# Kernel tuning notes

Measured on AMD Instinct MI355X. Metric: run time of the kernel, lower is better.

Reference implementation:

```python
import jax, jax.numpy as jnp
import numpy as np

N = 5000      # nodes per event (hardcoded in PFNet7.forward)
BIN = 100     # LSH bin_size
K = 16        # kNN per node within bin
SLOPE = 0.01  # LeakyReLU default negative slope


def _mlp(x, W1, b1, W2, b2, W3, b3):
    h = jax.nn.leaky_relu(x @ W1 + b1, SLOPE)
    h = jax.nn.leaky_relu(h @ W2 + b2, SLOPE)
    return h @ W3 + b3


def _build_graph_lsh(x, codebook):
    # x: [N, F]. Faithful vectorized version of GraphBuildingLSH (batch=1).
    n_bins = N // BIN                                   # 50
    mul = x @ codebook[:, : n_bins // 2]                # [N, 25]
    cmul = jnp.concatenate([mul, -mul], axis=-1)        # [N, 50]
    bin_idx = jnp.argmax(cmul, axis=-1)                 # [N]
    bins_split = jnp.argsort(bin_idx).reshape(n_bins, BIN)  # [nb, BIN]
    pts = x[bins_split]                                 # [nb, BIN, F]
    dm = jax.nn.sigmoid(jnp.einsum('pif,pjf->pij', pts, pts))  # [nb, BIN, BIN]
    vals, inds = jax.lax.top_k(dm, K)                   # [nb, BIN, K]
    src = jnp.broadcast_to(bins_split[:, :, None], inds.shape).reshape(-1)
    dst = jnp.take_along_axis(bins_split, inds.reshape(n_bins, -1), axis=1).reshape(-1)
    val = vals.reshape(-1)                              # [nb*BIN*K] = 80000 edges
    return src, dst, val


def _gcn_conv(x, W, b, src, dst, ew):
    # PyG GCNConv: add self-loops (weight 1), symmetric normalization, aggregate at col.
    n = x.shape[0]
    loop = jnp.arange(n)
    row = jnp.concatenate([src, loop])
    col = jnp.concatenate([dst, loop])
    w = jnp.concatenate([ew, jnp.ones((n,), x.dtype)])
    deg = jax.ops.segment_sum(w, col, num_segments=n)
    dis = jnp.where(deg > 0, deg ** -0.5, 0.0)
    norm = dis[row] * w * dis[col]
    h = x @ W
    out = jax.ops.segment_sum(norm[:, None] * h[row], col, num_segments=n)
    return out + b


def _graph_conv(x, Wrel, brel, Wroot, src, dst, ew):
    # PyG GraphConv(aggr='add'): lin_rel(sum_j w_ij x_j) + lin_root(x)
    agg = jax.ops.segment_sum(ew[:, None] * x[src], dst, num_segments=x.shape[0])
    return agg @ Wrel + brel + x @ Wroot


def setup_inputs() -> dict:
    key = jax.random.key(0)
    ks = jax.random.split(key, 24)
    f32 = jnp.float32
    d = {
        'x': jax.random.normal(ks[0], (N, 12), f32),
        'ygen_id': jax.random.normal(ks[1], (N, 6), f32),
        'ygen': jax.random.normal(ks[2], (N, 6), f32),
        'codebook': jax.random.normal(ks[3], (12, 100), f32),
        # nn1: 12 -> 125 -> 125 -> 12
        'nn1_W1': jax.random.normal(ks[4], (12, 125), f32) * 0.1,
        'nn1_b1': jnp.zeros((125,), f32),
        'nn1_W2': jax.random.normal(ks[5], (125, 125), f32) * 0.1,
        'nn1_b2': jnp.zeros((125,), f32),
        'nn1_W3': jax.random.normal(ks[6], (125, 12), f32) * 0.1,
        'nn1_b3': jnp.zeros((12,), f32),
        # GCNConv: 12 -> 32
        'gcn_W': jax.random.normal(ks[7], (12, 32), f32) * 0.1,
        'gcn_b': jnp.zeros((32,), f32),
        # GraphConv: 32 -> 32
        'gc_Wrel': jax.random.normal(ks[8], (32, 32), f32) * 0.1,
        'gc_brel': jnp.zeros((32,), f32),
        'gc_Wroot': jax.random.normal(ks[9], (32, 32), f32) * 0.1,
        # nn2: 32 -> 125 -> 125 -> 6
        'nn2_W1': jax.random.normal(ks[10], (32, 125), f32) * 0.1,
        'nn2_b1': jnp.zeros((125,), f32),
        'nn2_W2': jax.random.normal(ks[11], (125, 125), f32) * 0.1,
        'nn2_b2': jnp.zeros((125,), f32),
        'nn2_W3': jax.random.normal(ks[12], (125, 6), f32) * 0.1,
        'nn2_b3': jnp.zeros((6,), f32),
        # nn3: 38 -> 125 -> 125 -> 6
        'nn3_W1': jax.random.normal(ks[13], (38, 125), f32) * 0.1,
        'nn3_b1': jnp.zeros((125,), f32),
        'nn3_W2': jax.random.normal(ks[14], (125, 125), f32) * 0.1,
        'nn3_b2': jnp.zeros((125,), f32),
        'nn3_W3': jax.random.normal(ks[15], (125, 6), f32) * 0.1,
        'nn3_b3': jnp.zeros((6,), f32),
    }
    return d


def reference(x, ygen_id, ygen, codebook,
              nn1_W1, nn1_b1, nn1_W2, nn1_b2, nn1_W3, nn1_b3,
              gcn_W, gcn_b, gc_Wrel, gc_brel, gc_Wroot,
              nn2_W1, nn2_b1, nn2_W2, nn2_b2, nn2_W3, nn2_b3,
              nn3_W1, nn3_b1, nn3_W2, nn3_b2, nn3_W3, nn3_b3):
    h = _mlp(x, nn1_W1, nn1_b1, nn1_W2, nn1_b2, nn1_W3, nn1_b3)   # [N, 12]
    src, dst, ew = _build_graph_lsh(h, codebook)
    h = jax.nn.leaky_relu(h, SLOPE)
    h = _gcn_conv(h, gcn_W, gcn_b, src, dst, ew)                   # [N, 32]
    h = _graph_conv(h, gc_Wrel, gc_brel, gc_Wroot, src, dst, ew)
    h = jax.nn.leaky_relu(h, SLOPE)
    cand_ids = _mlp(h, nn2_W1, nn2_b1, nn2_W2, nn2_b2, nn2_W3, nn2_b3)
    cand_p4 = _mlp(jnp.concatenate([h, cand_ids], axis=-1),
                   nn3_W1, nn3_b1, nn3_W2, nn3_b2, nn3_W3, nn3_b3)
    return (cand_ids, cand_p4, ygen_id, ygen)
```

## Files before the change

kernel.cpp:

```cpp
#include <hip/hip_runtime.h>
#include <math.h>

#define NN 5000
#define NBINS 50
#define BINSZ 100
#define KNN 16
#define BPAD 104
#define MROWS 112
#define NB 20

typedef _Float16 half8 __attribute__((ext_vector_type(8)));

__device__ __forceinline__ float lrelu(float x){ return x >= 0.f ? x : 0.01f*x; }

__global__ __launch_bounds__(640) void nn1_kernel(
    const float* __restrict__ x,
    const float* __restrict__ W1, const float* __restrict__ b1,
    const float* __restrict__ W2, const float* __restrict__ b2,
    const float* __restrict__ W3, const float* __restrict__ b3,
    const float* __restrict__ cb,
    const float4* __restrict__ ygen_id4, const float4* __restrict__ ygen4,
    float4* __restrict__ out4,
    float* __restrict__ h_out, int* __restrict__ bin_idx)
{
    __shared__ __align__(16) float sW[18628];
    __shared__ __align__(16) float bufX[240];
    __shared__ __align__(16) float bufA[2500];
    __shared__ __align__(16) float bufB[2500];
    __shared__ __align__(16) float sCB[300];
    int tid = threadIdx.x;
    int n0 = blockIdx.x * NB;
    int g = tid >> 7, j = tid & 127;
    float acc[4];

    if (tid >= 576 && tid < 636) {
        int gI = blockIdx.x * 60 + (tid - 576);
        out4[15000 + gI] = (gI < 7500) ? ygen_id4[gI] : ygen4[gI - 7500];
    }
    if (tid < 60) {
        float4 v = ((const float4*)(x + n0 * 12))[tid];
        int e = tid * 4;
        bufX[(e % 12) * NB + (e / 12)] = v.x;
        bufX[((e + 1) % 12) * NB + ((e + 1) / 12)] = v.y;
        bufX[((e + 2) % 12) * NB + ((e + 2) / 12)] = v.z;
        bufX[((e + 3) % 12) * NB + ((e + 3) / 12)] = v.w;
    }
    if (tid >= 60 && tid < 360) {
        int t = tid - 60; int k = t / 25, c = t - k * 25;
        sCB[t] = cb[k * 100 + c];
    }
    for (int t = tid; t < 375; t += 640) ((float4*)sW)[t] = ((const float4*)W1)[t];
    for (int t = tid; t < 3906; t += 640) ((float4*)(sW + 1500))[t] = ((const float4*)W2)[t];
    if (tid == 636) sW[1500 + 15624] = W2[15624];
    for (int t = tid; t < 375; t += 640) ((float4*)(sW + 17128))[t] = ((const float4*)W3)[t];
    __syncthreads();

    if (j < 125) {
        float bj = b1[j];
        acc[0] = bj; acc[1] = bj; acc[2] = bj; acc[3] = bj;
        #pragma unroll
        for (int k = 0; k < 12; ++k) {
            float w = sW[k * 125 + j];
            float4 a = *(const float4*)&bufX[k * NB + g * 4];
            acc[0] += a.x * w; acc[1] += a.y * w; acc[2] += a.z * w; acc[3] += a.w * w;
        }
        #pragma unroll
        for (int n = 0; n < 4; ++n) bufA[j * NB + g * 4 + n] = lrelu(acc[n]);
    }
    __syncthreads();

    if (j < 125) {
        float bj = b2[j];
        acc[0] = bj; acc[1] = bj; acc[2] = bj; acc[3] = bj;
        #pragma unroll 25
        for (int k = 0; k < 125; ++k) {
            float w = sW[1500 + k * 125 + j];
            float4 a = *(const float4*)&bufA[k * NB + g * 4];
            acc[0] += a.x * w; acc[1] += a.y * w; acc[2] += a.z * w; acc[3] += a.w * w;
        }
        #pragma unroll
        for (int n = 0; n < 4; ++n) bufB[j * NB + g * 4 + n] = lrelu(acc[n]);
    }
    __syncthreads();

    if (j < 48) {
        int jj = j % 12, s = j / 12;
        float ps[4] = {0.f, 0.f, 0.f, 0.f};
        if (s < 3) {
            int k0 = s * 32;
            #pragma unroll
            for (int k = 0; k < 32; ++k) {
                float w = sW[17128 + (k0 + k) * 12 + jj];
                float4 a = *(const float4*)&bufB[(k0 + k) * NB + g * 4];
                ps[0] += a.x * w; ps[1] += a.y * w; ps[2] += a.z * w; ps[3] += a.w * w;
            }
        } else {
            #pragma unroll
            for (int k = 0; k < 29; ++k) {
                float w = sW[17128 + (96 + k) * 12 + jj];
                float4 a = *(const float4*)&bufB[(96 + k) * NB + g * 4];
                ps[0] += a.x * w; ps[1] += a.y * w; ps[2] += a.z * w; ps[3] += a.w * w;
            }
        }
        #pragma unroll
        for (int n = 0; n < 4; ++n) bufA[(s * 12 + jj) * NB + g * 4 + n] = ps[n];
    }
    __syncthreads();
    if (tid < 240) {
        int jj = tid / 20, n = tid % 20;
        float v = bufA[jj * NB + n] + bufA[(12 + jj) * NB + n]
                + bufA[(24 + jj) * NB + n] + bufA[(36 + jj) * NB + n] + b3[jj];
        h_out[(n0 + n) * 12 + jj] = v;
        bufB[jj * NB + n] = v;
    }
    __syncthreads();

    if (tid < 500) {
        int n = tid / 25, c = tid % 25;
        float m = 0.f;
        #pragma unroll
        for (int k = 0; k < 12; ++k) m += bufB[k * NB + n] * sCB[k * 25 + c];
        bufA[c * NB + n] = m;
    }
    __syncthreads();
    if (tid < NB) {
        int n = tid;
        float best = -INFINITY; int bi = 0;
        #pragma unroll
        for (int c = 0; c < 25; ++c) {
            float m = bufA[c * NB + n];
            if (m > best) { best = m; bi = c; }
        }
        #pragma unroll
        for (int c = 0; c < 25; ++c) {
            float m = -bufA[c * NB + n];
            if (m > best) { best = m; bi = c + 25; }
        }
        bin_idx[n0 + n] = bi;
    }
}

__global__ __launch_bounds__(640) void scatter_kernel(
    const int* __restrict__ bin_idx, int* __restrict__ order)
{
    __shared__ int sBI[NN];
    __shared__ int s_lt[10], s_eq[10];
    int tid = threadIdx.x, bb = blockIdx.x;
    for (int t = tid; t < NN / 4; t += 640) ((int4*)sBI)[t] = ((const int4*)bin_idx)[t];
    __syncthreads();
    int lane = tid & 63, w = tid >> 6;
    int start = w * 512;
    int end = (start + 512 > NN) ? NN : start + 512;
    int cnt_lt = 0, cnt_eq = 0;
    for (int base = start; base < end; base += 64) {
        int i = base + lane;
        int bi = (i < end) ? sBI[i] : 999;
        cnt_lt += __popcll(__ballot(bi < bb));
        cnt_eq += __popcll(__ballot(bi == bb));
    }
    if (lane == 0) { s_lt[w] = cnt_lt; s_eq[w] = cnt_eq; }
    __syncthreads();
    int offs = 0;
    #pragma unroll
    for (int w2 = 0; w2 < 10; ++w2) {
        offs += s_lt[w2];
        if (w2 < w) offs += s_eq[w2];
    }
    unsigned long long below = lane ? ((~0ULL) >> (64 - lane)) : 0ULL;
    for (int base = start; base < end; base += 64) {
        int i = base + lane;
        int bi = (i < end) ? sBI[i] : 999;
        unsigned long long m = __ballot(bi == bb);
        if (bi == bb) order[offs + __popcll(m & below)] = i;
        offs += __popcll(m);
    }
}

__global__ __launch_bounds__(640) void graph_kernel(
    const float* __restrict__ h, const int* __restrict__ order,
    const float* __restrict__ gcn_W, const float* __restrict__ gcn_b,
    float* __restrict__ gcn_n, float* __restrict__ agg_n)
{
    __shared__ _Float16 M[MROWS * BPAD];
    __shared__ float s_h[BINSZ * 12];
    __shared__ int   s_nodes[BINSZ];
    __shared__ float s_dis[BINSZ];
    __shared__ float s_w[12 * 32];
    __shared__ union {
        unsigned s_tv[200 * KNN];
        struct { float hWd[32 * BPAD]; float gcn[32 * BPAD]; } c;
    } U;
    int p = blockIdx.x, tid = threadIdx.x;

    if (tid < BINSZ) s_nodes[tid] = order[p * BINSZ + tid];
    for (int t = tid; t < MROWS * BPAD / 2; t += 640) ((int*)M)[t] = 0;
    if (tid < 384) s_w[tid] = gcn_W[tid];
    __syncthreads();
    for (int t = tid; t < BINSZ * 12; t += 640) {
        int i = t / 12, k = t - i * 12;
        s_h[t] = h[s_nodes[i] * 12 + k];
    }
    __syncthreads();

    if (tid < 200) {
        int row = tid >> 1, half = tid & 1;
        const float4* xp = (const float4*)&s_h[row * 12];
        float4 x0 = xp[0], x1 = xp[1], x2 = xp[2];
        unsigned tv[KNN];
        #pragma unroll
        for (int k = 0; k < KNN; ++k) tv[k] = 0u;
        int j0 = half * 50;
        for (int jj = 0; jj < 50; ++jj) {
            int jn = j0 + jj;
            const float4* ap = (const float4*)&s_h[jn * 12];
            float4 a0 = ap[0], a1 = ap[1], a2 = ap[2];
            float d = x0.x*a0.x + x0.y*a0.y + x0.z*a0.z + x0.w*a0.w
                    + x1.x*a1.x + x1.y*a1.y + x1.z*a1.z + x1.w*a1.w
                    + x2.x*a2.x + x2.y*a2.y + x2.z*a2.z + x2.w*a2.w;
            float v = 1.f / (1.f + expf(-d));
            unsigned key = (__float_as_uint(v) & 0xFFFFFF80u) | (unsigned)(127 - jn);
            if (key > tv[KNN - 1]) {
                unsigned ins = key;
                #pragma unroll
                for (int k = 0; k < KNN; ++k) {
                    bool gt = ins > tv[k];
                    unsigned mx = gt ? ins : tv[k];
                    unsigned mn = gt ? tv[k] : ins;
                    tv[k] = mx; ins = mn;
                }
            }
        }
        #pragma unroll
        for (int k = 0; k < KNN; ++k) U.s_tv[tid * KNN + k] = tv[k];
    }
    __syncthreads();

    if (tid < BINSZ) {
        int mbase = tid * 32;
        int ia = 0, ib = 0;
        #pragma unroll
        for (int k = 0; k < KNN; ++k) {
            unsigned av = U.s_tv[mbase + ia], bv = U.s_tv[mbase + 16 + ib];
            bool tA = av > bv;
            unsigned key = tA ? av : bv;
            ia += tA; ib += !tA;
            int ix = 127 - (int)(key & 127u);
            M[ix * BPAD + tid] = (_Float16)__uint_as_float(key & 0xFFFFFF80u);
        }
    }
    __syncthreads();
    if (tid < BINSZ) {
        float dsum = 1.0f;
        #pragma unroll 13
        for (int sc = 0; sc < 13; ++sc) {
            half8 m = *(const half8*)&M[tid * BPAD + sc * 8];
            dsum += (float)m[0] + (float)m[1] + (float)m[2] + (float)m[3]
                  + (float)m[4] + (float)m[5] + (float)m[6] + (float)m[7];
        }
        s_dis[tid] = 1.0f / sqrtf(dsum);
    }
    __syncthreads();

    if (tid < 256) {
        int c = tid >> 3, r = tid & 7;
        if (r < 4) U.c.hWd[c * BPAD + 100 + r] = 0.f;
        else       U.c.gcn[c * BPAD + 100 + (r - 4)] = 0.f;
    }
    for (int o = tid; o < BINSZ * 32; o += 640) {
        int s = o >> 5, c = o & 31;
        float a = 0.f;
        #pragma unroll
        for (int k = 0; k < 12; ++k) a += lrelu(s_h[s * 12 + k]) * s_w[k * 32 + c];
        U.c.hWd[c * BPAD + s] = s_dis[s] * a;
    }
    __syncthreads();

    {
        int c = tid / 20, dg = tid % 20;
        float acc5[5];
        #pragma unroll
        for (int r = 0; r < 5; ++r) acc5[r] = 0.f;
        for (int sc = 0; sc < 13; ++sc) {
            float4 hv0 = *(const float4*)&U.c.hWd[c * BPAD + sc * 8];
            float4 hv1 = *(const float4*)&U.c.hWd[c * BPAD + sc * 8 + 4];
            #pragma unroll
            for (int r = 0; r < 5; ++r) {
                int d = dg + 20 * r;
                half8 m = *(const half8*)&M[d * BPAD + sc * 8];
                acc5[r] += (float)m[0]*hv0.x + (float)m[1]*hv0.y + (float)m[2]*hv0.z + (float)m[3]*hv0.w
                         + (float)m[4]*hv1.x + (float)m[5]*hv1.y + (float)m[6]*hv1.z + (float)m[7]*hv1.w;
            }
        }
        float bc = gcn_b[c];
        #pragma unroll
        for (int r = 0; r < 5; ++r) {
            int d = dg + 20 * r;
            float gq = s_dis[d] * (acc5[r] + U.c.hWd[c * BPAD + d]) + bc;
            U.c.gcn[c * BPAD + d] = gq;
            gcn_n[s_nodes[d] * 32 + c] = gq;
        }
    }
    __syncthreads();
    {
        int c = tid / 20, dg = tid % 20;
        float acc5[5];
        #pragma unroll
        for (int r = 0; r < 5; ++r) acc5[r] = 0.f;
        for (int sc = 0; sc < 13; ++sc) {
            float4 hv0 = *(const float4*)&U.c.gcn[c * BPAD + sc * 8];
            float4 hv1 = *(const float4*)&U.c.gcn[c * BPAD + sc * 8 + 4];
            #pragma unroll
            for (int r = 0; r < 5; ++r) {
                int d = dg + 20 * r;
                half8 m = *(const half8*)&M[d * BPAD + sc * 8];
                acc5[r] += (float)m[0]*hv0.x + (float)m[1]*hv0.y + (float)m[2]*hv0.z + (float)m[3]*hv0.w
                         + (float)m[4]*hv1.x + (float)m[5]*hv1.y + (float)m[6]*hv1.z + (float)m[7]*hv1.w;
            }
        }
        #pragma unroll
        for (int r = 0; r < 5; ++r) {
            int d = dg + 20 * r;
            agg_n[s_nodes[d] * 32 + c] = acc5[r];
        }
    }
}

__global__ __launch_bounds__(640) void nn23_kernel(
    const float* __restrict__ gcn_n, const float* __restrict__ agg_n,
    const float* __restrict__ Wrel, const float* __restrict__ brel,
    const float* __restrict__ Wroot,
    const float* __restrict__ A1, const float* __restrict__ ab1,
    const float* __restrict__ A2, const float* __restrict__ ab2,
    const float* __restrict__ A3, const float* __restrict__ ab3,
    const float* __restrict__ B1, const float* __restrict__ bb1,
    const float* __restrict__ B2, const float* __restrict__ bb2,
    const float* __restrict__ B3, const float* __restrict__ bb3,
    float* __restrict__ out_ids, float* __restrict__ out_p4)
{
    __shared__ __align__(16) float sW[22428];
    __shared__ __align__(16) float sAG[640];
    __shared__ __align__(16) float sGC[640];
    __shared__ __align__(16) float bufC[760];
    __shared__ __align__(16) float bufA[2500];
    __shared__ __align__(16) float bufB[2500];
    int tid = threadIdx.x;
    int n0 = blockIdx.x * NB;
    int g = tid >> 7, j = tid & 127;
    float acc[4];

    if (tid < 160) {
        float4 va = ((const float4*)(agg_n + n0 * 32))[tid];
        float4 vg = ((const float4*)(gcn_n + n0 * 32))[tid];
        int e = tid * 4, n = e / 32, k = e % 32;
        sAG[k * NB + n] = va.x; sAG[(k+1) * NB + n] = va.y;
        sAG[(k+2) * NB + n] = va.z; sAG[(k+3) * NB + n] = va.w;
        sGC[k * NB + n] = vg.x; sGC[(k+1) * NB + n] = vg.y;
        sGC[(k+2) * NB + n] = vg.z; sGC[(k+3) * NB + n] = vg.w;
    }
    if (tid >= 160 && tid < 416) ((float4*)sW)[tid - 160] = ((const float4*)Wrel)[tid - 160];
    if (tid >= 416 && tid < 636) ((float4*)(sW + 1024))[tid - 416] = ((const float4*)Wroot)[tid - 416];
    if (tid < 36) ((float4*)(sW + 1024))[220 + tid] = ((const float4*)Wroot)[220 + tid];
    for (int t = tid; t < 1000; t += 640) ((float4*)(sW + 2048))[t] = ((const float4*)A1)[t];
    for (int t = tid; t < 3906; t += 640) ((float4*)(sW + 6048))[t] = ((const float4*)A2)[t];
    if (tid == 637) sW[6048 + 15624] = A2[15624];
    if (tid >= 416 && tid < 603) ((float4*)(sW + 21676))[tid - 416] = ((const float4*)A3)[tid - 416];
    if (tid == 638) { sW[21676 + 748] = A3[748]; sW[21676 + 749] = A3[749]; }
    __syncthreads();

    {
        int jc = tid / 20, n = tid % 20;
        float a = brel[jc];
        #pragma unroll
        for (int k = 0; k < 32; ++k)
            a += sAG[k * NB + n] * sW[k * 32 + jc] + sGC[k * NB + n] * sW[1024 + k * 32 + jc];
        bufC[jc * NB + n] = lrelu(a);
    }
    __syncthreads();

    if (j < 125) {
        float bj = ab1[j];
        acc[0] = bj; acc[1] = bj; acc[2] = bj; acc[3] = bj;
        #pragma unroll
        for (int k = 0; k < 32; ++k) {
            float w = sW[2048 + k * 125 + j];
            float4 a = *(const float4*)&bufC[k * NB + g * 4];
            acc[0] += a.x * w; acc[1] += a.y * w; acc[2] += a.z * w; acc[3] += a.w * w;
        }
        #pragma unroll
        for (int n = 0; n < 4; ++n) bufA[j * NB + g * 4 + n] = lrelu(acc[n]);
    }
    __syncthreads();

    if (j < 125) {
        float bj = ab2[j];
        acc[0] = bj; acc[1] = bj; acc[2] = bj; acc[3] = bj;
        #pragma unroll 25
        for (int k = 0; k < 125; ++k) {
            float w = sW[6048 + k * 125 + j];
            float4 a = *(const float4*)&bufA[k * NB + g * 4];
            acc[0] += a.x * w; acc[1] += a.y * w; acc[2] += a.z * w; acc[3] += a.w * w;
        }
        #pragma unroll
        for (int n = 0; n < 4; ++n) bufB[j * NB + g * 4 + n] = lrelu(acc[n]);
    }
    __syncthreads();

    if (j < 24) {
        int jj = j % 6, s = j / 6;
        float ps[4] = {0.f, 0.f, 0.f, 0.f};
        if (s < 3) {
            int k0 = s * 32;
            #pragma unroll
            for (int k = 0; k < 32; ++k) {
                float w = sW[21676 + (k0 + k) * 6 + jj];
                float4 a = *(const float4*)&bufB[(k0 + k) * NB + g * 4];
                ps[0] += a.x * w; ps[1] += a.y * w; ps[2] += a.z * w; ps[3] += a.w * w;
            }
        } else {
            #pragma unroll
            for (int k = 0; k < 29; ++k) {
                float w = sW[21676 + (96 + k) * 6 + jj];
                float4 a = *(const float4*)&bufB[(96 + k) * NB + g * 4];
                ps[0] += a.x * w; ps[1] += a.y * w; ps[2] += a.z * w; ps[3] += a.w * w;
            }
        }
        #pragma unroll
        for (int n = 0; n < 4; ++n) bufA[(s * 6 + jj) * NB + g * 4 + n] = ps[n];
    }
    __syncthreads();
    if (tid < 120) {
        int jj = tid / 20, n = tid % 20;
        float v = bufA[jj * NB + n] + bufA[(6 + jj) * NB + n]
                + bufA[(12 + jj) * NB + n] + bufA[(18 + jj) * NB + n] + ab3[jj];
        out_ids[(n0 + n) * 6 + jj] = v;
        bufC[(32 + jj) * NB + n] = v;
    }
    for (int t = tid; t < 1187; t += 640) ((float4*)sW)[t] = ((const float4*)B1)[t];
    if (tid == 600) { sW[4748] = B1[4748]; sW[4749] = B1[4749]; }
    for (int t = tid; t < 3906; t += 640) ((float4*)(sW + 4752))[t] = ((const float4*)B2)[t];
    if (tid == 601) sW[4752 + 15624] = B2[15624];
    if (tid >= 256 && tid < 443) ((float4*)(sW + 20380))[tid - 256] = ((const float4*)B3)[tid - 256];
    if (tid == 602) { sW[20380 + 748] = B3[748]; sW[20380 + 749] = B3[749]; }
    __syncthreads();

    if (j < 125) {
        float bj = bb1[j];
        acc[0] = bj; acc[1] = bj; acc[2] = bj; acc[3] = bj;
        #pragma unroll 19
        for (int k = 0; k < 38; ++k) {
            float w = sW[k * 125 + j];
            float4 a = *(const float4*)&bufC[k * NB + g * 4];
            acc[0] += a.x * w; acc[1] += a.y * w; acc[2] += a.z * w; acc[3] += a.w * w;
        }
        #pragma unroll
        for (int n = 0; n < 4; ++n) bufA[j * NB + g * 4 + n] = lrelu(acc[n]);
    }
    __syncthreads();

    if (j < 125) {
        float bj = bb2[j];
        acc[0] = bj; acc[1] = bj; acc[2] = bj; acc[3] = bj;
        #pragma unroll 25
        for (int k = 0; k < 125; ++k) {
            float w = sW[4752 + k * 125 + j];
            float4 a = *(const float4*)&bufA[k * NB + g * 4];
            acc[0] += a.x * w; acc[1] += a.y * w; acc[2] += a.z * w; acc[3] += a.w * w;
        }
        #pragma unroll
        for (int n = 0; n < 4; ++n) bufB[j * NB + g * 4 + n] = lrelu(acc[n]);
    }
    __syncthreads();

    if (j < 24) {
        int jj = j % 6, s = j / 6;
        float ps[4] = {0.f, 0.f, 0.f, 0.f};
        if (s < 3) {
            int k0 = s * 32;
            #pragma unroll
            for (int k = 0; k < 32; ++k) {
                float w = sW[20380 + (k0 + k) * 6 + jj];
                float4 a = *(const float4*)&bufB[(k0 + k) * NB + g * 4];
                ps[0] += a.x * w; ps[1] += a.y * w; ps[2] += a.z * w; ps[3] += a.w * w;
            }
        } else {
            #pragma unroll
            for (int k = 0; k < 29; ++k) {
                float w = sW[20380 + (96 + k) * 6 + jj];
                float4 a = *(const float4*)&bufB[(96 + k) * NB + g * 4];
                ps[0] += a.x * w; ps[1] += a.y * w; ps[2] += a.z * w; ps[3] += a.w * w;
            }
        }
        #pragma unroll
        for (int n = 0; n < 4; ++n) bufA[(s * 6 + jj) * NB + g * 4 + n] = ps[n];
    }
    __syncthreads();
    if (tid < 120) {
        int jj = tid / 20, n = tid % 20;
        float v = bufA[jj * NB + n] + bufA[(6 + jj) * NB + n]
                + bufA[(12 + jj) * NB + n] + bufA[(18 + jj) * NB + n] + bb3[jj];
        out_p4[(n0 + n) * 6 + jj] = v;
    }
}

extern "C" void kernel_launch(void* const* d_in, const int* in_sizes, int n_in,
                              void* d_out, int out_size, void* d_ws, size_t ws_size,
                              hipStream_t stream) {
    const float* x        = (const float*)d_in[0];
    const float* ygen_id  = (const float*)d_in[1];
    const float* ygen     = (const float*)d_in[2];
    const float* codebook = (const float*)d_in[3];
    const float* nn1_W1 = (const float*)d_in[4];  const float* nn1_b1 = (const float*)d_in[5];
    const float* nn1_W2 = (const float*)d_in[6];  const float* nn1_b2 = (const float*)d_in[7];
    const float* nn1_W3 = (const float*)d_in[8];  const float* nn1_b3 = (const float*)d_in[9];
    const float* gcn_W  = (const float*)d_in[10]; const float* gcn_b  = (const float*)d_in[11];
    const float* gc_Wrel = (const float*)d_in[12]; const float* gc_brel = (const float*)d_in[13];
    const float* gc_Wroot = (const float*)d_in[14];
    const float* nn2_W1 = (const float*)d_in[15]; const float* nn2_b1 = (const float*)d_in[16];
    const float* nn2_W2 = (const float*)d_in[17]; const float* nn2_b2 = (const float*)d_in[18];
    const float* nn2_W3 = (const float*)d_in[19]; const float* nn2_b3 = (const float*)d_in[20];
    const float* nn3_W1 = (const float*)d_in[21]; const float* nn3_b1 = (const float*)d_in[22];
    const float* nn3_W2 = (const float*)d_in[23]; const float* nn3_b2 = (const float*)d_in[24];
    const float* nn3_W3 = (const float*)d_in[25]; const float* nn3_b3 = (const float*)d_in[26];

    float* out = (float*)d_out;
    float* ws  = (float*)d_ws;

    float* h      = ws + 0;
    float* gcn_n  = ws + 60000;
    float* agg_n  = ws + 220000;
    int* bin_idx  = (int*)(ws + 380000);
    int* order    = (int*)(ws + 385000);

    nn1_kernel<<<NN / NB, 640, 0, stream>>>(
        x, nn1_W1, nn1_b1, nn1_W2, nn1_b2, nn1_W3, nn1_b3, codebook,
        (const float4*)ygen_id, (const float4*)ygen, (float4*)out,
        h, bin_idx);

    scatter_kernel<<<NBINS, 640, 0, stream>>>(bin_idx, order);

    graph_kernel<<<NBINS, 640, 0, stream>>>(h, order, gcn_W, gcn_b, gcn_n, agg_n);

    nn23_kernel<<<NN / NB, 640, 0, stream>>>(
        gcn_n, agg_n, gc_Wrel, gc_brel, gc_Wroot,
        nn2_W1, nn2_b1, nn2_W2, nn2_b2, nn2_W3, nn2_b3,
        nn3_W1, nn3_b1, nn3_W2, nn3_b2, nn3_W3, nn3_b3,
        out, out + 30000);
}
```

Measured before the change: 178.7 us.

## Shrink MLP tiles to 8 nodes and read weights directly from global/L2

Node tile size for the nn1 and nn23 MLP kernels drops from 20 to 8, with 256-thread blocks instead of 640, which launches 625 blocks. The per-block shared-memory staging of all weight matrices is removed, and weights are now read directly from global memory, relying on L1/L2 caching. This cuts the large LDS footprint and the serialized weight-load prologue so occupancy can rise. In exchange, each weight element is re-read from cache by more blocks, and weight reuse per load falls.

```diff
diff --git a/kernel.cpp b/kernel.cpp
--- a/kernel.cpp
+++ b/kernel.cpp
@@ -7,13 +7,13 @@
 #define KNN 16
 #define BPAD 104
 #define MROWS 112
-#define NB 20
+#define NB 8
 
 typedef _Float16 half8 __attribute__((ext_vector_type(8)));
 
 __device__ __forceinline__ float lrelu(float x){ return x >= 0.f ? x : 0.01f*x; }
 
-__global__ __launch_bounds__(640) void nn1_kernel(
+__global__ __launch_bounds__(256) void nn1_kernel(
     const float* __restrict__ x,
     const float* __restrict__ W1, const float* __restrict__ b1,
     const float* __restrict__ W2, const float* __restrict__ b2,
@@ -23,21 +23,19 @@
     float4* __restrict__ out4,
     float* __restrict__ h_out, int* __restrict__ bin_idx)
 {
-    __shared__ __align__(16) float sW[18628];
-    __shared__ __align__(16) float bufX[240];
-    __shared__ __align__(16) float bufA[2500];
-    __shared__ __align__(16) float bufB[2500];
+    __shared__ __align__(16) float bufX[96];
+    __shared__ __align__(16) float bufA[1000];
+    __shared__ __align__(16) float bufB[1000];
     __shared__ __align__(16) float sCB[300];
     int tid = threadIdx.x;
     int n0 = blockIdx.x * NB;
     int g = tid >> 7, j = tid & 127;
-    float acc[4];
-
-    if (tid >= 576 && tid < 636) {
-        int gI = blockIdx.x * 60 + (tid - 576);
+
+    if (tid >= 232) {
+        int gI = blockIdx.x * 24 + (tid - 232);
         out4[15000 + gI] = (gI < 7500) ? ygen_id4[gI] : ygen4[gI - 7500];
     }
-    if (tid < 60) {
+    if (tid < 24) {
         float4 v = ((const float4*)(x + n0 * 12))[tid];
         int e = tid * 4;
         bufX[(e % 12) * NB + (e / 12)] = v.x;
@@ -45,41 +43,37 @@
         bufX[((e + 2) % 12) * NB + ((e + 2) / 12)] = v.z;
         bufX[((e + 3) % 12) * NB + ((e + 3) / 12)] = v.w;
     }
-    if (tid >= 60 && tid < 360) {
-        int t = tid - 60; int k = t / 25, c = t - k * 25;
+    for (int t = tid; t < 300; t += 256) {
+        int k = t / 25, c = t - k * 25;
         sCB[t] = cb[k * 100 + c];
     }
-    for (int t = tid; t < 375; t += 640) ((float4*)sW)[t] = ((const float4*)W1)[t];
-    for (int t = tid; t < 3906; t += 640) ((float4*)(sW + 1500))[t] = ((const float4*)W2)[t];
-    if (tid == 636) sW[1500 + 15624] = W2[15624];
-    for (int t = tid; t < 375; t += 640) ((float4*)(sW + 17128))[t] = ((const float4*)W3)[t];
     __syncthreads();
 
     if (j < 125) {
         float bj = b1[j];
-        acc[0] = bj; acc[1] = bj; acc[2] = bj; acc[3] = bj;
+        float acc[4] = {bj, bj, bj, bj};
         #pragma unroll
         for (int k = 0; k < 12; ++k) {
-            float w = sW[k * 125 + j];
+            float w = W1[k * 125 + j];
             float4 a = *(const float4*)&bufX[k * NB + g * 4];
             acc[0] += a.x * w; acc[1] += a.y * w; acc[2] += a.z * w; acc[3] += a.w * w;
         }
-        #pragma unroll
-        for (int n = 0; n < 4; ++n) bufA[j * NB + g * 4 + n] = lrelu(acc[n]);
+        *(float4*)&bufA[j * NB + g * 4] =
+            make_float4(lrelu(acc[0]), lrelu(acc[1]), lrelu(acc[2]), lrelu(acc[3]));
     }
     __syncthreads();
 
     if (j < 125) {
         float bj = b2[j];
-        acc[0] = bj; acc[1] = bj; acc[2] = bj; acc[3] = bj;
-        #pragma unroll 25
+        float acc[4] = {bj, bj, bj, bj};
+        #pragma unroll 5
         for (int k = 0; k < 125; ++k) {
-            float w = sW[1500 + k * 125 + j];
+            float w = W2[k * 125 + j];
             float4 a = *(const float4*)&bufA[k * NB + g * 4];
             acc[0] += a.x * w; acc[1] += a.y * w; acc[2] += a.z * w; acc[3] += a.w * w;
         }
-        #pragma unroll
-        for (int n = 0; n < 4; ++n) bufB[j * NB + g * 4 + n] = lrelu(acc[n]);
+        *(float4*)&bufB[j * NB + g * 4] =
+            make_float4(lrelu(acc[0]), lrelu(acc[1]), lrelu(acc[2]), lrelu(acc[3]));
     }
     __syncthreads();
 
@@ -90,24 +84,23 @@
             int k0 = s * 32;
             #pragma unroll
             for (int k = 0; k < 32; ++k) {
-                float w = sW[17128 + (k0 + k) * 12 + jj];
+                float w = W3[(k0 + k) * 12 + jj];
                 float4 a = *(const float4*)&bufB[(k0 + k) * NB + g * 4];
                 ps[0] += a.x * w; ps[1] += a.y * w; ps[2] += a.z * w; ps[3] += a.w * w;
             }
         } else {
             #pragma unroll
             for (int k = 0; k < 29; ++k) {
-                float w = sW[17128 + (96 + k) * 12 + jj];
+                float w = W3[(96 + k) * 12 + jj];
                 float4 a = *(const float4*)&bufB[(96 + k) * NB + g * 4];
                 ps[0] += a.x * w; ps[1] += a.y * w; ps[2] += a.z * w; ps[3] += a.w * w;
             }
         }
-        #pragma unroll
-        for (int n = 0; n < 4; ++n) bufA[(s * 12 + jj) * NB + g * 4 + n] = ps[n];
-    }
-    __syncthreads();
-    if (tid < 240) {
-        int jj = tid / 20, n = tid % 20;
+        *(float4*)&bufA[(s * 12 + jj) * NB + g * 4] = make_float4(ps[0], ps[1], ps[2], ps[3]);
+    }
+    __syncthreads();
+    if (tid < 96) {
+        int jj = tid / NB, n = tid % NB;
         float v = bufA[jj * NB + n] + bufA[(12 + jj) * NB + n]
                 + bufA[(24 + jj) * NB + n] + bufA[(36 + jj) * NB + n] + b3[jj];
         h_out[(n0 + n) * 12 + jj] = v;
@@ -115,7 +108,7 @@
     }
     __syncthreads();
 
-    if (tid < 500) {
+    if (tid < 200) {
         int n = tid / 25, c = tid % 25;
         float m = 0.f;
         #pragma unroll
@@ -325,7 +318,7 @@
     }
 }
 
-__global__ __launch_bounds__(640) void nn23_kernel(
+__global__ __launch_bounds__(256) void nn23_kernel(
     const float* __restrict__ gcn_n, const float* __restrict__ agg_n,
     const float* __restrict__ Wrel, const float* __restrict__ brel,
     const float* __restrict__ Wroot,
@@ -337,18 +330,16 @@
     const float* __restrict__ B3, const float* __restrict__ bb3,
     float* __restrict__ out_ids, float* __restrict__ out_p4)
 {
-    __shared__ __align__(16) float sW[22428];
-    __shared__ __align__(16) float sAG[640];
-    __shared__ __align__(16) float sGC[640];
-    __shared__ __align__(16) float bufC[760];
-    __shared__ __align__(16) float bufA[2500];
-    __shared__ __align__(16) float bufB[2500];
+    __shared__ __align__(16) float sAG[256];
+    __shared__ __align__(16) float sGC[256];
+    __shared__ __align__(16) float bufC[304];
+    __shared__ __align__(16) float bufA[1000];
+    __shared__ __align__(16) float bufB[1000];
     int tid = threadIdx.x;
     int n0 = blockIdx.x * NB;
     int g = tid >> 7, j = tid & 127;
-    float acc[4];
-
-    if (tid < 160) {
+
+    if (tid < 64) {
         float4 va = ((const float4*)(agg_n + n0 * 32))[tid];
         float4 vg = ((const float4*)(gcn_n + n0 * 32))[tid];
         int e = tid * 4, n = e / 32, k = e % 32;
@@ -357,51 +348,43 @@
         sGC[k * NB + n] = vg.x; sGC[(k+1) * NB + n] = vg.y;
         sGC[(k+2) * NB + n] = vg.z; sGC[(k+3) * NB + n] = vg.w;
     }
-    if (tid >= 160 && tid < 416) ((float4*)sW)[tid - 160] = ((const float4*)Wrel)[tid - 160];
-    if (tid >= 416 && tid < 636) ((float4*)(sW + 1024))[tid - 416] = ((const float4*)Wroot)[tid - 416];
-    if (tid < 36) ((float4*)(sW + 1024))[220 + tid] = ((const float4*)Wroot)[220 + tid];
-    for (int t = tid; t < 1000; t += 640) ((float4*)(sW + 2048))[t] = ((const float4*)A1)[t];
-    for (int t = tid; t < 3906; t += 640) ((float4*)(sW + 6048))[t] = ((const float4*)A2)[t];
-    if (tid == 637) sW[6048 + 15624] = A2[15624];
-    if (tid >= 416 && tid < 603) ((float4*)(sW + 21676))[tid - 416] = ((const float4*)A3)[tid - 416];
-    if (tid == 638) { sW[21676 + 748] = A3[748]; sW[21676 + 749] = A3[749]; }
     __syncthreads();
 
     {
-        int jc = tid / 20, n = tid % 20;
+        int jc = tid >> 3, n = tid & 7;
         float a = brel[jc];
-        #pragma unroll
+        #pragma unroll 8
         for (int k = 0; k < 32; ++k)
-            a += sAG[k * NB + n] * sW[k * 32 + jc] + sGC[k * NB + n] * sW[1024 + k * 32 + jc];
+            a += sAG[k * NB + n] * Wrel[k * 32 + jc] + sGC[k * NB + n] * Wroot[k * 32 + jc];
         bufC[jc * NB + n] = lrelu(a);
     }
     __syncthreads();
 
     if (j < 125) {
         float bj = ab1[j];
-        acc[0] = bj; acc[1] = bj; acc[2] = bj; acc[3] = bj;
-        #pragma unroll
+        float acc[4] = {bj, bj, bj, bj};
+        #pragma unroll 8
         for (int k = 0; k < 32; ++k) {
-            float w = sW[2048 + k * 125 + j];
+            float w = A1[k * 125 + j];
             float4 a = *(const float4*)&bufC[k * NB + g * 4];
             acc[0] += a.x * w; acc[1] += a.y * w; acc[2] += a.z * w; acc[3] += a.w * w;
         }
-        #pragma unroll
-        for (int n = 0; n < 4; ++n) bufA[j * NB + g * 4 + n] = lrelu(acc[n]);
+        *(float4*)&bufA[j * NB + g * 4] =
+            make_float4(lrelu(acc[0]), lrelu(acc[1]), lrelu(acc[2]), lrelu(acc[3]));
     }
     __syncthreads();
 
     if (j < 125) {
         float bj = ab2[j];
-        acc[0] = bj; acc[1] = bj; acc[2] = bj; acc[3] = bj;
-        #pragma unroll 25
+        float acc[4] = {bj, bj, bj, bj};
+        #pragma unroll 5
         for (int k = 0; k < 125; ++k) {
-            float w = sW[6048 + k * 125 + j];
+            float w = A2[k * 125 + j];
             float4 a = *(const float4*)&bufA[k * NB + g * 4];
             acc[0] += a.x * w; acc[1] += a.y * w; acc[2] += a.z * w; acc[3] += a.w * w;
         }
-        #pragma unroll
-        for (int n = 0; n < 4; ++n) bufB[j * NB + g * 4 + n] = lrelu(acc[n]);
+        *(float4*)&bufB[j * NB + g * 4] =
+            make_float4(lrelu(acc[0]), lrelu(acc[1]), lrelu(acc[2]), lrelu(acc[3]));
     }
     __syncthreads();
 
@@ -412,62 +395,55 @@
             int k0 = s * 32;
             #pragma unroll
             for (int k = 0; k < 32; ++k) {
-                float w = sW[21676 + (k0 + k) * 6 + jj];
+                float w = A3[(k0 + k) * 6 + jj];
                 float4 a = *(const float4*)&bufB[(k0 + k) * NB + g * 4];
                 ps[0] += a.x * w; ps[1] += a.y * w; ps[2] += a.z * w; ps[3] += a.w * w;
             }
         } else {
             #pragma unroll
             for (int k = 0; k < 29; ++k) {
-                float w = sW[21676 + (96 + k) * 6 + jj];
+                float w = A3[(96 + k) * 6 + jj];
                 float4 a = *(const float4*)&bufB[(96 + k) * NB + g * 4];
                 ps[0] += a.x * w; ps[1] += a.y * w; ps[2] += a.z * w; ps[3] += a.w * w;
             }
         }
-        #pragma unroll
-        for (int n = 0; n < 4; ++n) bufA[(s * 6 + jj) * NB + g * 4 + n] = ps[n];
-    }
-    __syncthreads();
-    if (tid < 120) {
-        int jj = tid / 20, n = tid % 20;
+        *(float4*)&bufA[(s * 6 + jj) * NB + g * 4] = make_float4(ps[0], ps[1], ps[2], ps[3]);
+    }
+    __syncthreads();
+    if (tid < 48) {
+        int jj = tid / NB, n = tid % NB;
         float v = bufA[jj * NB + n] + bufA[(6 + jj) * NB + n]
                 + bufA[(12 + jj) * NB + n] + bufA[(18 + jj) * NB + n] + ab3[jj];
         out_ids[(n0 + n) * 6 + jj] = v;
         bufC[(32 + jj) * NB + n] = v;
     }
-    for (int t = tid; t < 1187; t += 640) ((float4*)sW)[t] = ((const float4*)B1)[t];
-    if (tid == 600) { sW[4748] = B1[4748]; sW[4749] = B1[4749]; }
-    for (int t = tid; t < 3906; t += 640) ((float4*)(sW + 4752))[t] = ((const float4*)B2)[t];
-    if (tid == 601) sW[4752 + 15624] = B2[15624];
-    if (tid >= 256 && tid < 443) ((float4*)(sW + 20380))[tid - 256] = ((const float4*)B3)[tid - 256];
-    if (tid == 602) { sW[20380 + 748] = B3[748]; sW[20380 + 749] = B3[749]; }
     __syncthreads();
 
     if (j < 125) {
         float bj = bb1[j];
-        acc[0] = bj; acc[1] = bj; acc[2] = bj; acc[3] = bj;
-        #pragma unroll 19
+        float acc[4] = {bj, bj, bj, bj};
+        #pragma unroll 2
         for (int k = 0; k < 38; ++k) {
-            float w = sW[k * 125 + j];
+            float w = B1[k * 125 + j];
             float4 a = *(const float4*)&bufC[k * NB + g * 4];
             acc[0] += a.x * w; acc[1] += a.y * w; acc[2] += a.z * w; acc[3] += a.w * w;
         }
-        #pragma unroll
-        for (int n = 0; n < 4; ++n) bufA[j * NB + g * 4 + n] = lrelu(acc[n]);
+        *(float4*)&bufA[j * NB + g * 4] =
+            make_float4(lrelu(acc[0]), lrelu(acc[1]), lrelu(acc[2]), lrelu(acc[3]));
     }
     __syncthreads();
 
     if (j < 125) {
         float bj = bb2[j];
-        acc[0] = bj; acc[1] = bj; acc[2] = bj; acc[3] = bj;
-        #pragma unroll 25
+        float acc[4] = {bj, bj, bj, bj};
+        #pragma unroll 5
         for (int k = 0; k < 125; ++k) {
-            float w = sW[4752 + k * 125 + j];
+            float w = B2[k * 125 + j];
             float4 a = *(const float4*)&bufA[k * NB + g * 4];
             acc[0] += a.x * w; acc[1] += a.y * w; acc[2] += a.z * w; acc[3] += a.w * w;
         }
-        #pragma unroll
-        for (int n = 0; n < 4; ++n) bufB[j * NB + g * 4 + n] = lrelu(acc[n]);
+        *(float4*)&bufB[j * NB + g * 4] =
+            make_float4(lrelu(acc[0]), lrelu(acc[1]), lrelu(acc[2]), lrelu(acc[3]));
     }
     __syncthreads();
 
@@ -478,24 +454,23 @@
             int k0 = s * 32;
             #pragma unroll
             for (int k = 0; k < 32; ++k) {
-                float w = sW[20380 + (k0 + k) * 6 + jj];
+                float w = B3[(k0 + k) * 6 + jj];
                 float4 a = *(const float4*)&bufB[(k0 + k) * NB + g * 4];
                 ps[0] += a.x * w; ps[1] += a.y * w; ps[2] += a.z * w; ps[3] += a.w * w;
             }
         } else {
             #pragma unroll
             for (int k = 0; k < 29; ++k) {
-                float w = sW[20380 + (96 + k) * 6 + jj];
+                float w = B3[(96 + k) * 6 + jj];
                 float4 a = *(const float4*)&bufB[(96 + k) * NB + g * 4];
                 ps[0] += a.x * w; ps[1] += a.y * w; ps[2] += a.z * w; ps[3] += a.w * w;
             }
         }
-        #pragma unroll
-        for (int n = 0; n < 4; ++n) bufA[(s * 6 + jj) * NB + g * 4 + n] = ps[n];
-    }
-    __syncthreads();
-    if (tid < 120) {
-        int jj = tid / 20, n = tid % 20;
+        *(float4*)&bufA[(s * 6 + jj) * NB + g * 4] = make_float4(ps[0], ps[1], ps[2], ps[3]);
+    }
+    __syncthreads();
+    if (tid < 48) {
+        int jj = tid / NB, n = tid % NB;
         float v = bufA[jj * NB + n] + bufA[(6 + jj) * NB + n]
                 + bufA[(12 + jj) * NB + n] + bufA[(18 + jj) * NB + n] + bb3[jj];
         out_p4[(n0 + n) * 6 + jj] = v;
@@ -531,7 +506,7 @@
     int* bin_idx  = (int*)(ws + 380000);
     int* order    = (int*)(ws + 385000);
 
-    nn1_kernel<<<NN / NB, 640, 0, stream>>>(
+    nn1_kernel<<<NN / NB, 256, 0, stream>>>(
         x, nn1_W1, nn1_b1, nn1_W2, nn1_b2, nn1_W3, nn1_b3, codebook,
         (const float4*)ygen_id, (const float4*)ygen, (float4*)out,
         h, bin_idx);
@@ -540,7 +515,7 @@
 
     graph_kernel<<<NBINS, 640, 0, stream>>>(h, order, gcn_W, gcn_b, gcn_n, agg_n);
 
-    nn23_kernel<<<NN / NB, 640, 0, stream>>>(
+    nn23_kernel<<<NN / NB, 256, 0, stream>>>(
         gcn_n, agg_n, gc_Wrel, gc_brel, gc_Wroot,
         nn2_W1, nn2_b1, nn2_W2, nn2_b2, nn2_W3, nn2_b3,
         nn3_W1, nn3_b1, nn3_W2, nn3_b2, nn3_W3, nn3_b3,
```

Measured after the change: 181.3 us. About the same (+1.5%).

## Fuse bin scatter into graph kernel by recomputing global sort ranks per block

Applied to the files above, without the earlier changes.

Removes the separate scatter kernel launch and the order buffer round-trip. Each graph block now loads all bin indices into shared memory (reusing the M buffer), counts every bin per wave with ballots, prefix-sums the counts into global stable ranks, and picks out the nodes that fall in its own slice of the sorted order. This saves a launch and a global sync, but every block repeats the full counting and ranking work, including loops of 50 ballots per chunk.

```diff
diff --git a/kernel.cpp b/kernel.cpp
--- a/kernel.cpp
+++ b/kernel.cpp
@@ -140,44 +140,9 @@
     }
 }
 
-__global__ __launch_bounds__(640) void scatter_kernel(
-    const int* __restrict__ bin_idx, int* __restrict__ order)
-{
-    __shared__ int sBI[NN];
-    __shared__ int s_lt[10], s_eq[10];
-    int tid = threadIdx.x, bb = blockIdx.x;
-    for (int t = tid; t < NN / 4; t += 640) ((int4*)sBI)[t] = ((const int4*)bin_idx)[t];
-    __syncthreads();
-    int lane = tid & 63, w = tid >> 6;
-    int start = w * 512;
-    int end = (start + 512 > NN) ? NN : start + 512;
-    int cnt_lt = 0, cnt_eq = 0;
-    for (int base = start; base < end; base += 64) {
-        int i = base + lane;
-        int bi = (i < end) ? sBI[i] : 999;
-        cnt_lt += __popcll(__ballot(bi < bb));
-        cnt_eq += __popcll(__ballot(bi == bb));
-    }
-    if (lane == 0) { s_lt[w] = cnt_lt; s_eq[w] = cnt_eq; }
-    __syncthreads();
-    int offs = 0;
-    #pragma unroll
-    for (int w2 = 0; w2 < 10; ++w2) {
-        offs += s_lt[w2];
-        if (w2 < w) offs += s_eq[w2];
-    }
-    unsigned long long below = lane ? ((~0ULL) >> (64 - lane)) : 0ULL;
-    for (int base = start; base < end; base += 64) {
-        int i = base + lane;
-        int bi = (i < end) ? sBI[i] : 999;
-        unsigned long long m = __ballot(bi == bb);
-        if (bi == bb) order[offs + __popcll(m & below)] = i;
-        offs += __popcll(m);
-    }
-}
-
 __global__ __launch_bounds__(640) void graph_kernel(
-    const float* __restrict__ h, const int* __restrict__ order,
+    const int* __restrict__ bin_idx,
+    const float* __restrict__ h,
     const float* __restrict__ gcn_W, const float* __restrict__ gcn_b,
     float* __restrict__ gcn_n, float* __restrict__ agg_n)
 {
@@ -186,15 +151,79 @@
     __shared__ int   s_nodes[BINSZ];
     __shared__ float s_dis[BINSZ];
     __shared__ float s_w[12 * 32];
+    __shared__ int wcb[10][50];
+    __shared__ int runl[10][50];
+    __shared__ int startb[50];
+    __shared__ int totb[50];
     __shared__ union {
         unsigned s_tv[200 * KNN];
         struct { float hWd[32 * BPAD]; float gcn[32 * BPAD]; } c;
     } U;
     int p = blockIdx.x, tid = threadIdx.x;
-
-    if (tid < BINSZ) s_nodes[tid] = order[p * BINSZ + tid];
+    int* sBI = (int*)M;
+
+    for (int t = tid; t < NN / 4; t += 640) ((int4*)sBI)[t] = ((const int4*)bin_idx)[t];
+    if (tid < 384) s_w[tid] = gcn_W[tid];
+    {
+        int w0 = tid >> 6, l0 = tid & 63;
+        if (l0 < 50) { wcb[w0][l0] = 0; runl[w0][l0] = 0; }
+    }
+    __syncthreads();
+
+    int lane = tid & 63, w = tid >> 6;
+    int st = w * 512;
+    int en = (st + 512 > NN) ? NN : st + 512;
+
+    for (int b = 0; b < NBINS; ++b) {
+        int c = 0;
+        for (int base = st; base < en; base += 64) {
+            int i = base + lane;
+            int bi = (i < en) ? sBI[i] : -1;
+            c += __popcll(__ballot(bi == b));
+        }
+        if (lane == 0) wcb[w][b] = c;
+    }
+    __syncthreads();
+
+    if (tid < NBINS) {
+        int tot = 0;
+        #pragma unroll
+        for (int w2 = 0; w2 < 10; ++w2) { int v = wcb[w2][tid]; wcb[w2][tid] = tot; tot += v; }
+        totb[tid] = tot;
+    }
+    __syncthreads();
+    if (tid == 0) {
+        int s = 0;
+        #pragma unroll
+        for (int b = 0; b < NBINS; ++b) { startb[b] = s; s += totb[b]; }
+    }
+    __syncthreads();
+
+    {
+        unsigned long long below = lane ? ((~0ULL) >> (64 - lane)) : 0ULL;
+        int lo = p * BINSZ;
+        for (int base = st; base < en; base += 64) {
+            int i = base + lane;
+            int bi = (i < en) ? sBI[i] : -1;
+            unsigned long long mym = 0ULL;
+            for (int b = 0; b < NBINS; ++b) {
+                unsigned long long mm = __ballot(bi == b);
+                if (bi == b) mym = mm;
+            }
+            if (bi >= 0) {
+                int rank = startb[bi] + wcb[w][bi] + runl[w][bi] + __popcll(mym & below);
+                int loc = rank - lo;
+                if (loc >= 0 && loc < BINSZ) s_nodes[loc] = i;
+            }
+            for (int b = 0; b < NBINS; ++b) {
+                unsigned long long mm = __ballot(bi == b);
+                if (lane == b) runl[w][b] += __popcll(mm);
+            }
+        }
+    }
+    __syncthreads();
+
     for (int t = tid; t < MROWS * BPAD / 2; t += 640) ((int*)M)[t] = 0;
-    if (tid < 384) s_w[tid] = gcn_W[tid];
     __syncthreads();
     for (int t = tid; t < BINSZ * 12; t += 640) {
         int i = t / 12, k = t - i * 12;
@@ -529,16 +558,13 @@
     float* gcn_n  = ws + 60000;
     float* agg_n  = ws + 220000;
     int* bin_idx  = (int*)(ws + 380000);
-    int* order    = (int*)(ws + 385000);
 
     nn1_kernel<<<NN / NB, 640, 0, stream>>>(
         x, nn1_W1, nn1_b1, nn1_W2, nn1_b2, nn1_W3, nn1_b3, codebook,
         (const float4*)ygen_id, (const float4*)ygen, (float4*)out,
         h, bin_idx);
 
-    scatter_kernel<<<NBINS, 640, 0, stream>>>(bin_idx, order);
-
-    graph_kernel<<<NBINS, 640, 0, stream>>>(h, order, gcn_W, gcn_b, gcn_n, agg_n);
+    graph_kernel<<<NBINS, 640, 0, stream>>>(bin_idx, h, gcn_W, gcn_b, gcn_n, agg_n);
 
     nn23_kernel<<<NN / NB, 640, 0, stream>>>(
         gcn_n, agg_n, gc_Wrel, gc_brel, gc_Wroot,
```

Result: slower. 263.5 us (+47.5%).

## Give each wavefront two nodes in the tail MLPs to remove block barriers

Applied to the files above, without the earlier changes.

The final MLP kernel is repartitioned so each of the 10 wavefronts owns two nodes end to end. Each lane computes two output columns (l and l+64) for both nodes, and the last-layer partial sums are reduced with cross-lane shuffles instead of shared memory. This removes most __syncthreads between layers, because only intra-wave data dependencies remain. In exchange, each thread does twice the column work with fewer nodes per weight load, which reduces reuse of the shared weights.

```diff
diff --git a/kernel.cpp b/kernel.cpp
--- a/kernel.cpp
+++ b/kernel.cpp
@@ -345,8 +345,8 @@
     __shared__ __align__(16) float bufB[2500];
     int tid = threadIdx.x;
     int n0 = blockIdx.x * NB;
-    int g = tid >> 7, j = tid & 127;
-    float acc[4];
+    int wv = tid >> 6, l = tid & 63;
+    int nc = wv * 2;
 
     if (tid < 160) {
         float4 va = ((const float4*)(agg_n + n0 * 32))[tid];
@@ -368,73 +368,82 @@
     __syncthreads();
 
     {
-        int jc = tid / 20, n = tid % 20;
+        int jc = l & 31, n = nc + (l >> 5);
         float a = brel[jc];
         #pragma unroll
         for (int k = 0; k < 32; ++k)
             a += sAG[k * NB + n] * sW[k * 32 + jc] + sGC[k * NB + n] * sW[1024 + k * 32 + jc];
         bufC[jc * NB + n] = lrelu(a);
     }
-    __syncthreads();
-
-    if (j < 125) {
-        float bj = ab1[j];
-        acc[0] = bj; acc[1] = bj; acc[2] = bj; acc[3] = bj;
+
+    {
+        float b0 = ab1[l];
+        float b1v = (l < 61) ? ab1[l + 64] : 0.f;
+        float a00 = b0, a01 = b0, a10 = b1v, a11 = b1v;
         #pragma unroll
         for (int k = 0; k < 32; ++k) {
-            float w = sW[2048 + k * 125 + j];
-            float4 a = *(const float4*)&bufC[k * NB + g * 4];
-            acc[0] += a.x * w; acc[1] += a.y * w; acc[2] += a.z * w; acc[3] += a.w * w;
-        }
-        #pragma unroll
-        for (int n = 0; n < 4; ++n) bufA[j * NB + g * 4 + n] = lrelu(acc[n]);
-    }
-    __syncthreads();
-
-    if (j < 125) {
-        float bj = ab2[j];
-        acc[0] = bj; acc[1] = bj; acc[2] = bj; acc[3] = bj;
+            float w0 = sW[2048 + k * 125 + l];
+            float w1 = sW[2048 + k * 125 + l + 64];
+            float2 a = *(const float2*)&bufC[k * NB + nc];
+            a00 += a.x * w0; a01 += a.y * w0;
+            a10 += a.x * w1; a11 += a.y * w1;
+        }
+        *(float2*)&bufA[l * NB + nc] = make_float2(lrelu(a00), lrelu(a01));
+        if (l < 61) *(float2*)&bufA[(l + 64) * NB + nc] = make_float2(lrelu(a10), lrelu(a11));
+    }
+
+    {
+        float b0 = ab2[l];
+        float b1v = (l < 61) ? ab2[l + 64] : 0.f;
+        float a00 = b0, a01 = b0, a10 = b1v, a11 = b1v;
         #pragma unroll 25
         for (int k = 0; k < 125; ++k) {
-            float w = sW[6048 + k * 125 + j];
-            float4 a = *(const float4*)&bufA[k * NB + g * 4];
-            acc[0] += a.x * w; acc[1] += a.y * w; acc[2] += a.z * w; acc[3] += a.w * w;
-        }
-        #pragma unroll
-        for (int n = 0; n < 4; ++n) bufB[j * NB + g * 4 + n] = lrelu(acc[n]);
-    }
-    __syncthreads();
-
-    if (j < 24) {
-        int jj = j % 6, s = j / 6;
-        float ps[4] = {0.f, 0.f, 0.f, 0.f};
-        if (s < 3) {
-            int k0 = s * 32;
-            #pragma unroll
-            for (int k = 0; k < 32; ++k) {
-                float w = sW[21676 + (k0 + k) * 6 + jj];
-                float4 a = *(const float4*)&bufB[(k0 + k) * NB + g * 4];
-                ps[0] += a.x * w; ps[1] += a.y * w; ps[2] += a.z * w; ps[3] += a.w * w;
-            }
-        } else {
-            #pragma unroll
-            for (int k = 0; k < 29; ++k) {
-                float w = sW[21676 + (96 + k) * 6 + jj];
-                float4 a = *(const float4*)&bufB[(96 + k) * NB + g * 4];
-                ps[0] += a.x * w; ps[1] += a.y * w; ps[2] += a.z * w; ps[3] += a.w * w;
-            }
-        }
-        #pragma unroll
-        for (int n = 0; n < 4; ++n) bufA[(s * 6 + jj) * NB + g * 4 + n] = ps[n];
-    }
-    __syncthreads();
-    if (tid < 120) {
-        int jj = tid / 20, n = tid % 20;
-        float v = bufA[jj * NB + n] + bufA[(6 + jj) * NB + n]
-                + bufA[(12 + jj) * NB + n] + bufA[(18 + jj) * NB + n] + ab3[jj];
-        out_ids[(n0 + n) * 6 + jj] = v;
-        bufC[(32 + jj) * NB + n] = v;
-    }
+            float w0 = sW[6048 + k * 125 + l];
+            float w1 = sW[6048 + k * 125 + l + 64];
+            float2 a = *(const float2*)&bufA[k * NB + nc];
+            a00 += a.x * w0; a01 += a.y * w0;
+            a10 += a.x * w1; a11 += a.y * w1;
+        }
+        *(float2*)&bufB[l * NB + nc] = make_float2(lrelu(a00), lrelu(a01));
+        if (l < 61) *(float2*)&bufB[(l + 64) * NB + nc] = make_float2(lrelu(a10), lrelu(a11));
+    }
+
+    {
+        float p0 = 0.f, p1 = 0.f;
+        if (l < 24) {
+            int jj = l % 6, s = l / 6;
+            if (s < 3) {
+                int k0 = s * 32;
+                #pragma unroll
+                for (int k = 0; k < 32; ++k) {
+                    float wt = sW[21676 + (k0 + k) * 6 + jj];
+                    float2 a = *(const float2*)&bufB[(k0 + k) * NB + nc];
+                    p0 += a.x * wt; p1 += a.y * wt;
+                }
+            } else {
+                #pragma unroll
+                for (int k = 0; k < 29; ++k) {
+                    float wt = sW[21676 + (96 + k) * 6 + jj];
+                    float2 a = *(const float2*)&bufB[(96 + k) * NB + nc];
+                    p0 += a.x * wt; p1 += a.y * wt;
+                }
+            }
+        }
+        float q0a = __shfl(p0, l + 6),  q1a = __shfl(p1, l + 6);
+        float q0b = __shfl(p0, l + 12), q1b = __shfl(p1, l + 12);
+        float q0c = __shfl(p0, l + 18), q1c = __shfl(p1, l + 18);
+        if (l < 6) {
+            float bj = ab3[l];
+            float v0 = p0 + q0a + q0b + q0c + bj;
+            float v1 = p1 + q1a + q1b + q1c + bj;
+            out_ids[(n0 + nc) * 6 + l] = v0;
+            out_ids[(n0 + nc + 1) * 6 + l] = v1;
+            bufC[(32 + l) * NB + nc] = v0;
+            bufC[(32 + l) * NB + nc + 1] = v1;
+        }
+    }
+
+    __syncthreads();
     for (int t = tid; t < 1187; t += 640) ((float4*)sW)[t] = ((const float4*)B1)[t];
     if (tid == 600) { sW[4748] = B1[4748]; sW[4749] = B1[4749]; }
     for (int t = tid; t < 3906; t += 640) ((float4*)(sW + 4752))[t] = ((const float4*)B2)[t];
@@ -443,62 +452,67 @@
     if (tid == 602) { sW[20380 + 748] = B3[748]; sW[20380 + 749] = B3[749]; }
     __syncthreads();
 
-    if (j < 125) {
-        float bj = bb1[j];
-        acc[0] = bj; acc[1] = bj; acc[2] = bj; acc[3] = bj;
+    {
+        float b0 = bb1[l];
+        float b1v = (l < 61) ? bb1[l + 64] : 0.f;
+        float a00 = b0, a01 = b0, a10 = b1v, a11 = b1v;
         #pragma unroll 19
         for (int k = 0; k < 38; ++k) {
-            float w = sW[k * 125 + j];
-            float4 a = *(const float4*)&bufC[k * NB + g * 4];
-            acc[0] += a.x * w; acc[1] += a.y * w; acc[2] += a.z * w; acc[3] += a.w * w;
-        }
-        #pragma unroll
-        for (int n = 0; n < 4; ++n) bufA[j * NB + g * 4 + n] = lrelu(acc[n]);
-    }
-    __syncthreads();
-
-    if (j < 125) {
-        float bj = bb2[j];
-        acc[0] = bj; acc[1] = bj; acc[2] = bj; acc[3] = bj;
+            float w0 = sW[k * 125 + l];
+            float w1 = sW[k * 125 + l + 64];
+            float2 a = *(const float2*)&bufC[k * NB + nc];
+            a00 += a.x * w0; a01 += a.y * w0;
+            a10 += a.x * w1; a11 += a.y * w1;
+        }
+        *(float2*)&bufA[l * NB + nc] = make_float2(lrelu(a00), lrelu(a01));
+        if (l < 61) *(float2*)&bufA[(l + 64) * NB + nc] = make_float2(lrelu(a10), lrelu(a11));
+    }
+
+    {
+        float b0 = bb2[l];
+        float b1v = (l < 61) ? bb2[l + 64] : 0.f;
+        float a00 = b0, a01 = b0, a10 = b1v, a11 = b1v;
         #pragma unroll 25
         for (int k = 0; k < 125; ++k) {
-            float w = sW[4752 + k * 125 + j];
-            float4 a = *(const float4*)&bufA[k * NB + g * 4];
-            acc[0] += a.x * w; acc[1] += a.y * w; acc[2] += a.z * w; acc[3] += a.w * w;
-        }
-        #pragma unroll
-        for (int n = 0; n < 4; ++n) bufB[j * NB + g * 4 + n] = lrelu(acc[n]);
-    }
-    __syncthreads();
-
-    if (j < 24) {
-        int jj = j % 6, s = j / 6;
-        float ps[4] = {0.f, 0.f, 0.f, 0.f};
-        if (s < 3) {
-            int k0 = s * 32;
-            #pragma unroll
-            for (int k = 0; k < 32; ++k) {
-                float w = sW[20380 + (k0 + k) * 6 + jj];
-                float4 a = *(const float4*)&bufB[(k0 + k) * NB + g * 4];
-                ps[0] += a.x * w; ps[1] += a.y * w; ps[2] += a.z * w; ps[3] += a.w * w;
-            }
-        } else {
-            #pragma unroll
-            for (int k = 0; k < 29; ++k) {
-                float w = sW[20380 + (96 + k) * 6 + jj];
-                float4 a = *(const float4*)&bufB[(96 + k) * NB + g * 4];
-                ps[0] += a.x * w; ps[1] += a.y * w; ps[2] += a.z * w; ps[3] += a.w * w;
-            }
-        }
-        #pragma unroll
-        for (int n = 0; n < 4; ++n) bufA[(s * 6 + jj) * NB + g * 4 + n] = ps[n];
-    }
-    __syncthreads();
-    if (tid < 120) {
-        int jj = tid / 20, n = tid % 20;
-        float v = bufA[jj * NB + n] + bufA[(6 + jj) * NB + n]
-                + bufA[(12 + jj) * NB + n] + bufA[(18 + jj) * NB + n] + bb3[jj];
-        out_p4[(n0 + n) * 6 + jj] = v;
+            float w0 = sW[4752 + k * 125 + l];
+            float w1 = sW[4752 + k * 125 + l + 64];
+            float2 a = *(const float2*)&bufA[k * NB + nc];
+            a00 += a.x * w0; a01 += a.y * w0;
+            a10 += a.x * w1; a11 += a.y * w1;
+        }
+        *(float2*)&bufB[l * NB + nc] = make_float2(lrelu(a00), lrelu(a01));
+        if (l < 61) *(float2*)&bufB[(l + 64) * NB + nc] = make_float2(lrelu(a10), lrelu(a11));
+    }
+
+    {
+        float p0 = 0.f, p1 = 0.f;
+        if (l < 24) {
+            int jj = l % 6, s = l / 6;
+            if (s < 3) {
+                int k0 = s * 32;
+                #pragma unroll
+                for (int k = 0; k < 32; ++k) {
+                    float wt = sW[20380 + (k0 + k) * 6 + jj];
+                    float2 a = *(const float2*)&bufB[(k0 + k) * NB + nc];
+                    p0 += a.x * wt; p1 += a.y * wt;
+                }
+            } else {
+                #pragma unroll
+                for (int k = 0; k < 29; ++k) {
+                    float wt = sW[20380 + (96 + k) * 6 + jj];
+                    float2 a = *(const float2*)&bufB[(96 + k) * NB + nc];
+                    p0 += a.x * wt; p1 += a.y * wt;
+                }
+            }
+        }
+        float q0a = __shfl(p0, l + 6),  q1a = __shfl(p1, l + 6);
+        float q0b = __shfl(p0, l + 12), q1b = __shfl(p1, l + 12);
+        float q0c = __shfl(p0, l + 18), q1c = __shfl(p1, l + 18);
+        if (l < 6) {
+            float bj = bb3[l];
+            out_p4[(n0 + nc) * 6 + l]     = p0 + q0a + q0b + q0c + bj;
+            out_p4[(n0 + nc + 1) * 6 + l] = p1 + q1a + q1b + q1c + bj;
+        }
     }
 }
 
```

Result: no change. 181.4 us (+1.5%).
